# Kernel optimization log

Measured on AMD Instinct MI355X. Metric: run time of the kernel, lower is better.

Reference implementation:

```python
import jax, jax.numpy as jnp
import numpy as np

SEQ, D_IN, H, C, B = 256, 1, 512, 10, 2048


def setup_inputs() -> dict:
    key = jax.random.key(0)
    ks = jax.random.split(key, 10)
    std = 1.0 / H
    def w(k, shape, s):
        return (jax.random.normal(k, shape, dtype=jnp.float32) * s)
    inp = {
        "x": jax.random.normal(ks[0], (B, SEQ), dtype=jnp.float32),
        "wgx": w(ks[1], (H, D_IN), std),
        "wix": w(ks[2], (H, D_IN), std),
        "wfx": w(ks[3], (H, D_IN), std),
        "wox": w(ks[4], (H, D_IN), std),
        "wgh": w(ks[5], (H, H), std),
        "wih": w(ks[6], (H, H), std),
        "wfh": w(ks[7], (H, H), std),
        "woh": w(ks[8], (H, H), std),
        "bg": jnp.zeros((H, 1), jnp.float32),
        "bi": jnp.zeros((H, 1), jnp.float32),
        "bf": jnp.ones((H, 1), jnp.float32),
        "bo": jnp.zeros((H, 1), jnp.float32),
        "wph": w(ks[9], (C, H), 1e-4),
        "bp": jnp.zeros((C, 1), jnp.float32),
        "h_init": jnp.zeros((H, 1), jnp.float32),
        "c_init": jnp.zeros((H, 1), jnp.float32),
    }
    return inp


def reference(x, wgx, wix, wfx, wox, wgh, wih, wfh, woh,
              bg, bi, bf, bo, wph, bp, h_init, c_init):
    batch = x.shape[0]
    hid = wgh.shape[0]
    # initial states broadcast to [H, B] so the scan carry has a fixed shape
    h0 = jnp.broadcast_to(h_init, (hid, batch))
    c0 = jnp.broadcast_to(c_init, (hid, batch))
    xs = x.T[:, None, :]  # [S, 1, B]: xt per step is [1, B]

    def step(carry, xt):
        ht, ct = carry
        gt = jnp.tanh(wgx @ xt + wgh @ ht + bg)
        it = jax.nn.sigmoid(wix @ xt + wih @ ht + bi)
        ft = jax.nn.sigmoid(wfx @ xt + wfh @ ht + bf)
        ot = jax.nn.sigmoid(wox @ xt + woh @ ht + bo)
        ct = gt * it + ct * ft
        ht = jnp.tanh(ct) * ot
        return (ht, ct), None

    (ht, _), _ = jax.lax.scan(step, (h0, c0), xs)
    return (wph @ ht + bp).T  # [B, C]
```

## Files before the change

### kernel.cpp

```cpp
#include <hip/hip_runtime.h>
#include <math.h>

#define HID   512
#define SEQL  256
#define BATCH 2048
#define NCLS  10
#define NB    16
#define H8S   552

typedef _Float16 f16x8 __attribute__((ext_vector_type(8)));
typedef _Float16 f16x4 __attribute__((ext_vector_type(4)));
typedef _Float16 f16x2 __attribute__((ext_vector_type(2)));
typedef float    f32x4 __attribute__((ext_vector_type(4)));
typedef int      i32x4 __attribute__((ext_vector_type(4)));
typedef int      i32x8 __attribute__((ext_vector_type(8)));
typedef long     i64;
typedef long     i64x2 __attribute__((ext_vector_type(2)));

__device__ __forceinline__ float fsig(float v)  { return 1.f / (1.f + __expf(-v)); }
__device__ __forceinline__ float ftanh(float v) { return 1.f - 2.f / (1.f + __expf(2.f * v)); }

__device__ __forceinline__ unsigned q4(float y) {
    const unsigned s = (y < 0.f) ? 8u : 0u;
    const float a = fabsf(y);
    const unsigned c = a < 0.25f ? 0u : a < 0.75f ? 1u : a < 1.25f ? 2u :
                       a < 1.75f ? 3u : a < 2.5f  ? 4u : a < 3.5f  ? 5u :
                       a < 5.0f  ? 6u : 7u;
    return s | c;
}

__global__ void pack_g(const float* __restrict__ wg, uint4* __restrict__ wqg)
{
    const int idx = blockIdx.x * 256 + threadIdx.x;
    const int lane = idx & 63;
    const int h  = (idx >> 6) & 1;
    const int pi = (idx >> 7) & 3;
    const int sc = (idx >> 9) & 3;
    const int wv = idx >> 11;
    const int j = 16 * (wv + 8 * pi) + (lane & 15);
    unsigned dw[4];
    #pragma unroll
    for (int d = 0; d < 4; d++) {
        float f[4];
        #pragma unroll
        for (int e = 0; e < 4; e++) {
            const int v = 4 * d + e;
            const int k = (4 * sc + 2 * h + (v >> 3)) * 32 + (lane >> 4) * 8 + (v & 7);
            f[e] = wg[j * HID + k] * 128.f;
        }
        int pk = __builtin_amdgcn_cvt_pk_fp8_f32(f[0], f[1], 0, false);
        pk     = __builtin_amdgcn_cvt_pk_fp8_f32(f[2], f[3], pk, true);
        dw[d] = (unsigned)pk;
    }
    wqg[idx] = make_uint4(dw[0], dw[1], dw[2], dw[3]);
}

__global__ void pack_ifo(const float* __restrict__ wi, const float* __restrict__ wf,
                         const float* __restrict__ wo, i32x4* __restrict__ wq4)
{
    const int idx = blockIdx.x * 256 + threadIdx.x;
    const int lane = idx & 63, blk = idx >> 6;
    const int t12 = blk % 12, r = blk / 12;
    const int sc = r & 3, wv = r >> 2;
    const int gt = t12 >> 2, pi = t12 & 3;
    const int j = 16 * (wv + 8 * pi) + (lane & 15);
    const int kbase = 128 * sc + (lane >> 4) * 32;
    const float* w = (gt == 0) ? wi : (gt == 1) ? wf : wo;
    int dw[4];
    #pragma unroll
    for (int d = 0; d < 4; d++) {
        unsigned u = 0;
        #pragma unroll
        for (int by = 0; by < 4; by++) {
            const int e0 = 8 * d + 2 * by;
            const unsigned c0 = q4(w[j * HID + kbase + e0]     * 1024.f);
            const unsigned c1 = q4(w[j * HID + kbase + e0 + 1] * 1024.f);
            u |= (c0 | (c1 << 4)) << (8 * by);
        }
        dw[d] = (int)u;
    }
    wq4[idx] = (i32x4){dw[0], dw[1], dw[2], dw[3]};
}

__device__ __forceinline__ void mma8a(f32x4& c, i64 a, i64 b) {
    asm volatile("v_mfma_f32_16x16x32_fp8_fp8 %0, %1, %2, %0"
                 : "+a"(c) : "v"(a), "v"(b));
}
__device__ __forceinline__ void mma4a(f32x4& c, i32x4 a, i32x8 b) {
    asm volatile("v_mfma_f32_16x16x128_f8f6f4 %0, %1, %2, %0 cbsz:4"
                 : "+a"(c) : "v"(a), "v"(b));
}
__device__ __forceinline__ i32x8 ld_h128(const char* p) {
    union { i64 q[4]; i32x8 v; } u;
    u.q[0] = *(const i64*)(p);
    u.q[1] = *(const i64*)(p + 8);
    u.q[2] = *(const i64*)(p + 16);
    u.q[3] = *(const i64*)(p + 24);
    return u.v;
}

__global__ __launch_bounds__(512, 1) void lstm_mfma(
    const float* __restrict__ x,
    const uint4* __restrict__ wqg, const i32x4* __restrict__ wq4,
    const float* __restrict__ wgx, const float* __restrict__ wix,
    const float* __restrict__ wfx, const float* __restrict__ wox,
    const float* __restrict__ bg,  const float* __restrict__ bi,
    const float* __restrict__ bf_, const float* __restrict__ bo,
    const float* __restrict__ wph, const float* __restrict__ bp,
    const float* __restrict__ h_init, const float* __restrict__ c_init,
    float* __restrict__ out)
{
    __shared__ __align__(16) char     h8s[2][NB * H8S];
    __shared__ float x_s[NB][SEQL + 1];
    __shared__ __align__(16) _Float16 hfin[NB][HID];

    const int tid  = threadIdx.x;
    const int lane = tid & 63;
    const int wv   = tid >> 6;
    const int col  = lane & 15;
    const int kq   = lane >> 4;
    const int b0   = blockIdx.x * NB;
    const int gbase = wv * 2048 + lane;
    const int qbase = wv * 3072 + lane;

    for (int i = tid; i < NB * SEQL; i += 512)
        x_s[i >> 8][i & 255] = x[(b0 + (i >> 8)) * SEQL + (i & 255)];

    for (int i = tid; i < 2 * NB * H8S; i += 512) {
        const int b = i / (NB * H8S), k = (i % (NB * H8S)) % H8S;
        const float v = (b == 0 && k < HID) ? h_init[k] * 128.f : 0.f;
        const int pk = __builtin_amdgcn_cvt_pk_fp8_f32(v, 0.f, 0, false);
        ((char*)h8s)[i] = (char)(pk & 0xff);
    }

    const int j00 = 16 * wv + 4 * kq;
    f32x4 creg[4];
    #pragma unroll
    for (int pi = 0; pi < 4; pi++) creg[pi] = *(const f32x4*)&c_init[j00 + 128 * pi];

    unsigned sv[16];
    {
        const float* gxp[4] = {wgx, wix, wfx, wox};
        const float* bpt[4] = {bg, bi, bf_, bo};
        #pragma unroll
        for (int a = 0; a < 16; a++) {
            const int pi = (a < 4) ? a : ((a - 4) & 3);
            const int gs = (a < 4) ? 0 : 1 + ((a - 4) >> 2);
            const int j  = 16 * (wv + 8 * pi) + col;
            const float sc  = (a < 4) ? 16384.f : 131072.f;
            f16x2 pr;
            pr[0] = (_Float16)(gxp[gs][j] * sc);
            pr[1] = (_Float16)(bpt[gs][j] * sc * (1.f / 256.f));
            sv[a] = (kq == 0) ? __builtin_bit_cast(unsigned, pr) : 0u;
        }
    }

    __syncthreads();

    uint4 GpA[4], GpB[4];
    i32x4 QL[6], QH[6];
    #pragma unroll
    for (int pi = 0; pi < 4; pi++) {
        GpA[pi] = wqg[gbase + (pi * 2 + 0) * 64];
        GpB[pi] = wqg[gbase + (pi * 2 + 1) * 64];
    }
    #pragma unroll
    for (int q6 = 0; q6 < 6; q6++) {
        QL[q6] = wq4[qbase + q6 * 64];
        QH[q6] = wq4[qbase + (6 + q6) * 64];
    }

    int toff = 0;

    #pragma unroll 1
    for (int t = 0; t < SEQL; t++) {
        const int rb = t & 1, wb = rb ^ 1;
        const char* hb8 = &h8s[rb][col * H8S];

        asm volatile("" : "+v"(toff));
        const uint4* __restrict__ wqg_t = wqg + toff;
        const i32x4* __restrict__ wq4_t = wq4 + toff;

        f16x8 Bs = {};
        if (kq == 0) { Bs[0] = (_Float16)x_s[col][t]; Bs[1] = (_Float16)256.f; }
        f32x4 acc[16];
        #pragma unroll
        for (int a = 0; a < 16; a++) {
            const f16x2 pr = __builtin_bit_cast(f16x2, sv[a]);
            f16x8 F = {};
            F[0] = pr[0]; F[1] = pr[1];
            acc[a] = __builtin_amdgcn_mfma_f32_16x16x32_f16(
                F, Bs, (f32x4){0.f, 0.f, 0.f, 0.f}, 0, 0, 0);
        }

        #pragma unroll
        for (int sc = 0; sc < 4; sc++) {
            const int scn = (sc + 1) & 3;
            {
                const i64 Bm0 = *(const i64*)(hb8 + (4 * sc + 0) * 32 + kq * 8);
                const i64 Bm1 = *(const i64*)(hb8 + (4 * sc + 1) * 32 + kq * 8);
                #pragma unroll
                for (int pi = 0; pi < 4; pi++) {
                    const i64x2 gv = __builtin_bit_cast(i64x2, GpA[pi]);
                    mma8a(acc[pi], gv.x, Bm0);
                    mma8a(acc[pi], gv.y, Bm1);
                }
            }
            #pragma unroll
            for (int pi = 0; pi < 4; pi++)
                GpA[pi] = wqg_t[gbase + (scn * 8 + pi * 2 + 0) * 64];
            const i32x8 Bv = ld_h128(hb8 + sc * 128 + kq * 32);
            #pragma unroll
            for (int q6 = 0; q6 < 6; q6++)
                mma4a(acc[4 + q6], QL[q6], Bv);
            #pragma unroll
            for (int q6 = 0; q6 < 6; q6++)
                QL[q6] = wq4_t[qbase + (scn * 12 + q6) * 64];
            {
                const i64 Bm2 = *(const i64*)(hb8 + (4 * sc + 2) * 32 + kq * 8);
                const i64 Bm3 = *(const i64*)(hb8 + (4 * sc + 3) * 32 + kq * 8);
                #pragma unroll
                for (int pi = 0; pi < 4; pi++) {
                    const i64x2 gv = __builtin_bit_cast(i64x2, GpB[pi]);
                    mma8a(acc[pi], gv.x, Bm2);
                    mma8a(acc[pi], gv.y, Bm3);
                }
            }
            #pragma unroll
            for (int pi = 0; pi < 4; pi++)
                GpB[pi] = wqg_t[gbase + (scn * 8 + pi * 2 + 1) * 64];
            #pragma unroll
            for (int q6 = 0; q6 < 6; q6++)
                mma4a(acc[10 + q6], QH[q6], Bv);
            #pragma unroll
            for (int q6 = 0; q6 < 6; q6++)
                QH[q6] = wq4_t[qbase + (scn * 12 + 6 + q6) * 64];
        }

        asm volatile("s_nop 7\n\ts_nop 7"
                     : "+a"(acc[12]), "+a"(acc[13]), "+a"(acc[14]), "+a"(acc[15]));

        const float S14 = 1.f / 16384.f, S17 = 1.f / 131072.f;
        #pragma unroll
        for (int pi = 0; pi < 4; pi++) {
            const int j0 = j00 + 128 * pi;
            float hr[4];
            #pragma unroll
            for (int r = 0; r < 4; r++) {
                const float g  = ftanh(acc[pi][r]      * S14);
                const float ii = fsig (acc[4 + pi][r]  * S17);
                const float ff = fsig (acc[8 + pi][r]  * S17);
                const float oo = fsig (acc[12 + pi][r] * S17);
                const float cc = fmaf(g, ii, creg[pi][r] * ff);
                creg[pi][r] = cc;
                hr[r] = ftanh(cc) * oo;
            }
            int pk = __builtin_amdgcn_cvt_pk_fp8_f32(hr[0] * 128.f, hr[1] * 128.f, 0, false);
            pk     = __builtin_amdgcn_cvt_pk_fp8_f32(hr[2] * 128.f, hr[3] * 128.f, pk, true);
            *(unsigned*)&h8s[wb][col * H8S + j0] = (unsigned)pk;
            if (t == SEQL - 1) {
                f16x4 hv;
                #pragma unroll
                for (int r = 0; r < 4; r++) hv[r] = (_Float16)hr[r];
                *(f16x4*)&hfin[col][j0] = hv;
            }
        }
        __syncthreads();
    }

    if (tid < NB * NCLS) {
        const int c = tid / NCLS, cls = tid - c * NCLS;
        float s = bp[cls];
        for (int k = 0; k < HID; k++)
            s = fmaf(wph[cls * HID + k], (float)hfin[c][k], s);
        out[(b0 + c) * NCLS + cls] = s;
    }
}

extern "C" void kernel_launch(void* const* d_in, const int* in_sizes, int n_in,
                              void* d_out, int out_size, void* d_ws, size_t ws_size,
                              hipStream_t stream)
{
    const float* x   = (const float*)d_in[0];
    const float* wgx = (const float*)d_in[1];
    const float* wix = (const float*)d_in[2];
    const float* wfx = (const float*)d_in[3];
    const float* wox = (const float*)d_in[4];
    const float* wgh = (const float*)d_in[5];
    const float* wih = (const float*)d_in[6];
    const float* wfh = (const float*)d_in[7];
    const float* woh = (const float*)d_in[8];
    const float* bg  = (const float*)d_in[9];
    const float* bi  = (const float*)d_in[10];
    const float* bf  = (const float*)d_in[11];
    const float* bo  = (const float*)d_in[12];
    const float* wph = (const float*)d_in[13];
    const float* bp  = (const float*)d_in[14];
    const float* h0  = (const float*)d_in[15];
    const float* c0  = (const float*)d_in[16];
    float* out = (float*)d_out;

    char* ws = (char*)d_ws;
    uint4* wqg = (uint4*)ws;
    i32x4* wq4 = (i32x4*)(ws + (256u << 10));

    pack_g  <<<dim3(64), dim3(256), 0, stream>>>(wgh, wqg);
    pack_ifo<<<dim3(96), dim3(256), 0, stream>>>(wih, wfh, woh, wq4);
    lstm_mfma<<<dim3(BATCH / NB), dim3(512), 0, stream>>>(
        x, wqg, wq4, wgx, wix, wfx, wox, bg, bi, bf, bo, wph, bp, h0, c0, out);
}
```

Baseline: 2.761 ms.

## Park cell state and input-projection constants in AGPRs, share one G-weight buffer

Moves the per-thread cell state and the packed input/bias scalars into accumulation registers through explicit accvgpr read/write asm, and merges the two gate-weight prefetch buffers (GpA/GpB) into a single reused buffer. The aim is to lower architectural VGPR pressure, which could avoid spills or allow more waves. In exchange, the GpB half of the weights is now loaded just before it is consumed, so less of that load latency is hidden, and every step pays extra accvgpr move instructions.

Result: faster. 2.381 ms (-13.7%).

```diff
diff --git a/kernel.cpp b/kernel.cpp
--- a/kernel.cpp
+++ b/kernel.cpp
@@ -19,6 +19,19 @@
 
 __device__ __forceinline__ float fsig(float v)  { return 1.f / (1.f + __expf(-v)); }
 __device__ __forceinline__ float ftanh(float v) { return 1.f - 2.f / (1.f + __expf(2.f * v)); }
+
+__device__ __forceinline__ void agw(float& a, float v) {
+    asm volatile("v_accvgpr_write_b32 %0, %1" : "=a"(a) : "v"(v));
+}
+__device__ __forceinline__ float agr(const float& a) {
+    float r; asm volatile("v_accvgpr_read_b32 %0, %1" : "=v"(r) : "a"(a)); return r;
+}
+__device__ __forceinline__ void agwu(unsigned& a, unsigned v) {
+    asm volatile("v_accvgpr_write_b32 %0, %1" : "=a"(a) : "v"(v));
+}
+__device__ __forceinline__ unsigned agru(const unsigned& a) {
+    unsigned r; asm volatile("v_accvgpr_read_b32 %0, %1" : "=v"(r) : "a"(a)); return r;
+}
 
 __device__ __forceinline__ unsigned q4(float y) {
     const unsigned s = (y < 0.f) ? 8u : 0u;
@@ -134,11 +147,16 @@
     }
 
     const int j00 = 16 * wv + 4 * kq;
-    f32x4 creg[4];
-    #pragma unroll
-    for (int pi = 0; pi < 4; pi++) creg[pi] = *(const f32x4*)&c_init[j00 + 128 * pi];
-
-    unsigned sv[16];
+
+    float cra[16];
+    #pragma unroll
+    for (int pi = 0; pi < 4; pi++) {
+        const f32x4 cv = *(const f32x4*)&c_init[j00 + 128 * pi];
+        #pragma unroll
+        for (int r = 0; r < 4; r++) agw(cra[pi * 4 + r], cv[r]);
+    }
+
+    unsigned sva[16];
     {
         const float* gxp[4] = {wgx, wix, wfx, wox};
         const float* bpt[4] = {bg, bi, bf_, bo};
@@ -151,19 +169,16 @@
             f16x2 pr;
             pr[0] = (_Float16)(gxp[gs][j] * sc);
             pr[1] = (_Float16)(bpt[gs][j] * sc * (1.f / 256.f));
-            sv[a] = (kq == 0) ? __builtin_bit_cast(unsigned, pr) : 0u;
+            agwu(sva[a], (kq == 0) ? __builtin_bit_cast(unsigned, pr) : 0u);
         }
     }
 
     __syncthreads();
 
-    uint4 GpA[4], GpB[4];
+    uint4 Gp[4];
     i32x4 QL[6], QH[6];
     #pragma unroll
-    for (int pi = 0; pi < 4; pi++) {
-        GpA[pi] = wqg[gbase + (pi * 2 + 0) * 64];
-        GpB[pi] = wqg[gbase + (pi * 2 + 1) * 64];
-    }
+    for (int pi = 0; pi < 4; pi++) Gp[pi] = wqg[gbase + (pi * 2 + 0) * 64];
     #pragma unroll
     for (int q6 = 0; q6 < 6; q6++) {
         QL[q6] = wq4[qbase + q6 * 64];
@@ -186,7 +201,7 @@
         f32x4 acc[16];
         #pragma unroll
         for (int a = 0; a < 16; a++) {
-            const f16x2 pr = __builtin_bit_cast(f16x2, sv[a]);
+            const f16x2 pr = __builtin_bit_cast(f16x2, agru(sva[a]));
             f16x8 F = {};
             F[0] = pr[0]; F[1] = pr[1];
             acc[a] = __builtin_amdgcn_mfma_f32_16x16x32_f16(
@@ -201,14 +216,14 @@
                 const i64 Bm1 = *(const i64*)(hb8 + (4 * sc + 1) * 32 + kq * 8);
                 #pragma unroll
                 for (int pi = 0; pi < 4; pi++) {
-                    const i64x2 gv = __builtin_bit_cast(i64x2, GpA[pi]);
+                    const i64x2 gv = __builtin_bit_cast(i64x2, Gp[pi]);
                     mma8a(acc[pi], gv.x, Bm0);
                     mma8a(acc[pi], gv.y, Bm1);
                 }
             }
             #pragma unroll
             for (int pi = 0; pi < 4; pi++)
-                GpA[pi] = wqg_t[gbase + (scn * 8 + pi * 2 + 0) * 64];
+                Gp[pi] = wqg_t[gbase + (sc * 8 + pi * 2 + 1) * 64];
             const i32x8 Bv = ld_h128(hb8 + sc * 128 + kq * 32);
             #pragma unroll
             for (int q6 = 0; q6 < 6; q6++)
@@ -221,14 +236,14 @@
                 const i64 Bm3 = *(const i64*)(hb8 + (4 * sc + 3) * 32 + kq * 8);
                 #pragma unroll
                 for (int pi = 0; pi < 4; pi++) {
-                    const i64x2 gv = __builtin_bit_cast(i64x2, GpB[pi]);
+                    const i64x2 gv = __builtin_bit_cast(i64x2, Gp[pi]);
                     mma8a(acc[pi], gv.x, Bm2);
                     mma8a(acc[pi], gv.y, Bm3);
                 }
             }
             #pragma unroll
             for (int pi = 0; pi < 4; pi++)
-                GpB[pi] = wqg_t[gbase + (scn * 8 + pi * 2 + 1) * 64];
+                Gp[pi] = wqg_t[gbase + (scn * 8 + pi * 2 + 0) * 64];
             #pragma unroll
             for (int q6 = 0; q6 < 6; q6++)
                 mma4a(acc[10 + q6], QH[q6], Bv);
@@ -251,8 +266,9 @@
                 const float ii = fsig (acc[4 + pi][r]  * S17);
                 const float ff = fsig (acc[8 + pi][r]  * S17);
                 const float oo = fsig (acc[12 + pi][r] * S17);
-                const float cc = fmaf(g, ii, creg[pi][r] * ff);
-                creg[pi][r] = cc;
+                const float cold = agr(cra[pi * 4 + r]);
+                const float cc = fmaf(g, ii, cold * ff);
+                agw(cra[pi * 4 + r], cc);
                 hr[r] = ftanh(cc) * oo;
             }
             int pk = __builtin_amdgcn_cvt_pk_fp8_f32(hr[0] * 128.f, hr[1] * 128.f, 0, false);
```
